# Performance work log

Measured on AMD Instinct MI355X. Metric: run time of the kernel, lower is better.

## Reference

```python
import jax, jax.numpy as jnp
import numpy as np

INPUT_DIM = 64
LATENT_DIM = 512
K = 32
BATCH = 262144


def xavier_uniform(key, shape):
    fan_out, fan_in = shape
    limit = float(np.sqrt(6.0 / (fan_in + fan_out)))
    return jax.random.uniform(key, shape, jnp.float32, -limit, limit)


def setup_inputs() -> dict:
    key = jax.random.key(0)
    kx, ke, kd = jax.random.split(key, 3)
    x = jax.random.normal(kx, (BATCH, INPUT_DIM), dtype=jnp.float32)
    enc_W = xavier_uniform(ke, (LATENT_DIM, INPUT_DIM))  # torch Linear weight layout [out, in]
    enc_b = jnp.zeros((LATENT_DIM,), jnp.float32)
    dec_W = xavier_uniform(kd, (INPUT_DIM, LATENT_DIM))
    dec_b = jnp.zeros((INPUT_DIM,), jnp.float32)
    return {"x": x, "enc_W": enc_W, "enc_b": enc_b, "dec_W": dec_W, "dec_b": dec_b}


def reference(x, enc_W, enc_b, dec_W, dec_b):
    # encode: linear -> relu -> top-k mask
    z = jax.nn.relu(x @ enc_W.T + enc_b)                 # [B, LATENT_DIM]
    vals, idx = jax.lax.top_k(z, K)                      # [B, K]
    rows = jnp.arange(z.shape[0])[:, None]               # [B, 1]
    z_sparse = jnp.zeros_like(z).at[rows, idx].set(vals) # scatter top-k back
    # decode
    x_hat = z_sparse @ dec_W.T + dec_b                   # [B, INPUT_DIM]
    return x_hat, z_sparse
```

## Files before the change

### kernel.cpp

```cpp
#include <hip/hip_runtime.h>


#define BATCH 262144
#define IND   64
#define LAT   512
#define TOPK  32
#define RPB   128
#define TR    32
#define NTT   (RPB / TR)
#define CCAP  128
#define EPSC  4.2e-3f
#define NB    32
#define NBPAD 36

typedef __attribute__((ext_vector_type(8))) short short8;
typedef __attribute__((ext_vector_type(4))) float f32x4;

__device__ __forceinline__ unsigned short f2bf(float f) {
  unsigned u = __float_as_uint(f);
  unsigned r = ((u >> 16) & 1u) + 0x7FFFu;
  return (unsigned short)((u + r) >> 16);
}
__device__ __forceinline__ float bfbits2f(unsigned short s) {
  return __uint_as_float(((unsigned)s) << 16);
}
__device__ __forceinline__ float edgef(int t) {
  return __uint_as_float((unsigned)(1888 + t) << 19);
}
__device__ __forceinline__ short8 pack8(float4 a, float4 b) {
  short8 r;
  r[0] = (short)f2bf(a.x); r[1] = (short)f2bf(a.y);
  r[2] = (short)f2bf(a.z); r[3] = (short)f2bf(a.w);
  r[4] = (short)f2bf(b.x); r[5] = (short)f2bf(b.y);
  r[6] = (short)f2bf(b.z); r[7] = (short)f2bf(b.w);
  return r;
}
__device__ __forceinline__ void split8(const float* p, short8& h, short8& l) {
  #pragma unroll
  for (int i = 0; i < 8; i++) {
    float v = p[i];
    unsigned short hb = f2bf(v);
    float r = v - bfbits2f(hb);
    h[i] = (short)hb;
    l[i] = (short)f2bf(r);
  }
}
__device__ __forceinline__ float exact_dot64(const float* __restrict__ wr,
                                             const float* xr) {
  float4 W[16];
  #pragma unroll
  for (int i = 0; i < 16; i++) W[i] = *(const float4*)(wr + 4*i);
  float s = 0.0f;
  #pragma unroll
  for (int i = 0; i < 16; i++) {
    const float4 xv = *(const float4*)(xr + 4*i);
    s = fmaf(xv.x, W[i].x, s);
    s = fmaf(xv.y, W[i].y, s);
    s = fmaf(xv.z, W[i].z, s);
    s = fmaf(xv.w, W[i].w, s);
  }
  return s;
}

__global__ __launch_bounds__(256, 2)
void sae_fused(const float* __restrict__ xg,
               const float* __restrict__ encW,
               const float* __restrict__ encB,
               const float* __restrict__ decW,
               const float* __restrict__ decB,
               float* __restrict__ out_xhat,
               float* __restrict__ out_z)
{
  __shared__ union {
    unsigned       hist[TR][NBPAD];
    unsigned       fb[256];
    unsigned short cidx[TR][CCAP];
  } hc;
  __shared__ unsigned short zsp[TR][520];
  __shared__ float    xtile[TR][68];
  __shared__ float    rowlo[TR];
  __shared__ float    xabs[TR];
  __shared__ float    xlo0[TR];
  __shared__ float    xinvw[TR];
  __shared__ float    xwid[TR];
  __shared__ int      ccnt[TR];
  __shared__ int      degen[TR];
  __shared__ int      wmax_i;
  __shared__ int      fbmask;

  const int tid  = threadIdx.x;
  const int w    = tid >> 6;
  const int lane = tid & 63;
  const int c    = lane & 15;
  const int q    = lane >> 4;

  if (tid == 0) wmax_i = 0;
  __syncthreads();

  short8 beh[8][2];
  float  lmax = 0.0f;
  #pragma unroll
  for (int n = 0; n < 8; n++)
    #pragma unroll
    for (int ks = 0; ks < 2; ks++) {
      const float* p = encW + (size_t)(128*w + 16*n + c)*IND + 32*ks + 8*q;
      float4 a = *(const float4*)p, b = *(const float4*)(p + 4);
      lmax = fmaxf(lmax, fmaxf(fmaxf(fabsf(a.x), fabsf(a.y)), fmaxf(fabsf(a.z), fabsf(a.w))));
      lmax = fmaxf(lmax, fmaxf(fmaxf(fabsf(b.x), fabsf(b.y)), fmaxf(fabsf(b.z), fabsf(b.w))));
      beh[n][ks] = pack8(a, b);
    }
  atomicMax(&wmax_i, __float_as_int(lmax));

  float ebias[8];
  #pragma unroll
  for (int n = 0; n < 8; n++) ebias[n] = encB[128*w + 16*n + c];
  const float dbias = decB[16*w + c];
  __syncthreads();
  const float wmaxf = __int_as_float(wmax_i);

  #pragma unroll 1
  for (int t = 0; t < NTT; t++) {
    const int rowbase = blockIdx.x * RPB + t * TR;

    {
      uint4 z4 = {0,0,0,0};
      uint4* hp = (uint4*)&hc.hist[0][0];
      hp[tid] = z4;
      if (tid < 32) hp[256 + tid] = z4;
      uint4* zp = (uint4*)&zsp[0][0];
      #pragma unroll
      for (int i = 0; i < 8; i++) zp[tid + 256*i] = z4;
      if (tid < 32) zp[2048 + tid] = z4;
      if (tid < TR) { ccnt[tid] = 0; degen[tid] = 0; }
      if (tid == 0) fbmask = 0;
    }
    {
      const int row = tid >> 3, sub = tid & 7;
      const f32x4* gp = (const f32x4*)(xg + (size_t)(rowbase + row)*IND) + 2*sub;
      f32x4 a = __builtin_nontemporal_load(gp);
      f32x4 b = __builtin_nontemporal_load(gp + 1);
      *(f32x4*)&xtile[row][8*sub]     = a;
      *(f32x4*)&xtile[row][8*sub + 4] = b;
      float s  = fabsf(a.x)+fabsf(a.y)+fabsf(a.z)+fabsf(a.w)
               + fabsf(b.x)+fabsf(b.y)+fabsf(b.z)+fabsf(b.w);
      float s2 = a.x*a.x+a.y*a.y+a.z*a.z+a.w*a.w
               + b.x*b.x+b.y*b.y+b.z*b.z+b.w*b.w;
      s  += __shfl_xor(s, 1);  s  += __shfl_xor(s, 2);  s  += __shfl_xor(s, 4);
      s2 += __shfl_xor(s2, 1); s2 += __shfl_xor(s2, 2); s2 += __shfl_xor(s2, 4);
      if (sub == 0) {
        xabs[row] = s;
        const float sig = 0.058926f * sqrtf(s2);
        xlo0[row]  = fmaxf(0.7f * sig, edgef(1));
        xwid[row]  = (2.5f / (float)NB) * sig;
        xinvw[row] = (float)NB / fmaxf(2.5f * sig, 1e-20f);
      }
    }
    __syncthreads();

    f32x4 acc[2][8];
    #pragma unroll
    for (int m2 = 0; m2 < 2; m2++)
      #pragma unroll
      for (int n = 0; n < 8; n++) acc[m2][n] = (f32x4){0.f,0.f,0.f,0.f};

    #pragma unroll
    for (int m2 = 0; m2 < 2; m2++) {
      const float* xr = &xtile[16*m2 + c][0];
      short8 a0h, a0l, a1h, a1l;
      split8(xr + 8*q,      a0h, a0l);
      split8(xr + 32 + 8*q, a1h, a1l);
      #pragma unroll
      for (int n = 0; n < 8; n++) {
        acc[m2][n] = __builtin_amdgcn_mfma_f32_16x16x32_bf16(a0h, beh[n][0], acc[m2][n], 0,0,0);
        acc[m2][n] = __builtin_amdgcn_mfma_f32_16x16x32_bf16(a0l, beh[n][0], acc[m2][n], 0,0,0);
        acc[m2][n] = __builtin_amdgcn_mfma_f32_16x16x32_bf16(a1h, beh[n][1], acc[m2][n], 0,0,0);
        acc[m2][n] = __builtin_amdgcn_mfma_f32_16x16x32_bf16(a1l, beh[n][1], acc[m2][n], 0,0,0);
      }
    }
    {
      float flo[2][4], fiw[2][4];
      #pragma unroll
      for (int m2 = 0; m2 < 2; m2++)
        #pragma unroll
        for (int r = 0; r < 4; r++) {
          flo[m2][r] = xlo0[16*m2 + 4*q + r];
          fiw[m2][r] = xinvw[16*m2 + 4*q + r];
        }
      #pragma unroll
      for (int m2 = 0; m2 < 2; m2++)
        #pragma unroll
        for (int n = 0; n < 8; n++)
          #pragma unroll
          for (int r = 0; r < 4; r++) {
            float v = fmaxf(acc[m2][n][r] + ebias[n], 0.0f);
            acc[m2][n][r] = v;
            if (v >= flo[m2][r]) {
              const int row = 16*m2 + 4*q + r;
              int k = (int)((v - flo[m2][r]) * fiw[m2][r]);
              k = min(k, NB-1);
              atomicAdd(&hc.hist[row][k], 1u);
            }
          }
    }
    __syncthreads();

    #pragma unroll 1
    for (int rr = 0; rr < 8; rr++) {
      const int row = 8*w + rr;
      uint4 h = {0,0,0,0};
      if (lane < 8) h = *(const uint4*)&hc.hist[row][4*lane];
      int T = (int)(h.x + h.y + h.z + h.w);
      int I = T;
      #pragma unroll
      for (int d = 1; d < 8; d <<= 1) {
        int t2 = __shfl_down(I, d);
        if (lane + d < 8) I += t2;
      }
      const int I0 = __shfl(I, 0);
      if (I0 < TOPK) {
        if (lane == 0) atomicOr(&fbmask, (int)(1u << row));
      } else {
        unsigned long long msk = __ballot(I >= TOPK);
        const int ls = __popcll(msk) - 1;
        const int Il = __shfl(I, ls);
        const int hx = __shfl((int)h.x, ls);
        const int hy = __shfl((int)h.y, ls);
        const int hz = __shfl((int)h.z, ls);
        const int s1 = Il - hx, s2 = s1 - hy, s3 = s2 - hz;
        const int t8 = (s3 >= TOPK) ? 4*ls+3 : (s2 >= TOPK) ? 4*ls+2
                     : (s1 >= TOPK) ? 4*ls+1 : 4*ls;
        if (lane == 0) {
          const float eps2 = EPSC * wmaxf * xabs[row] + 1e-7f;
          rowlo[row] = fmaxf(xlo0[row] + (float)t8 * xwid[row] - 2.0f*eps2, 1e-30f);
        }
      }
    }
    __syncthreads();

    if (fbmask) {
      unsigned* fb = &hc.fb[0];
      unsigned fbm = (unsigned)fbmask;
      while (fbm) {
        const int R = (int)__ffs(fbm) - 1;
        fbm &= fbm - 1;
        fb[tid] = 0;
        __syncthreads();
        if ((lane >> 4) == ((R >> 2) & 3)) {
          const int m2R = R >> 4, rR = R & 3;
          #pragma unroll
          for (int m2 = 0; m2 < 2; m2++)
            #pragma unroll
            for (int r = 0; r < 4; r++)
              if (m2 == m2R && r == rR) {
                #pragma unroll
                for (int n = 0; n < 8; n++) {
                  float v = acc[m2][n][r];
                  int k8 = (int)(__float_as_uint(v) >> 19) - 1888;
                  k8 = max(0, min(255, k8));
                  atomicAdd(&fb[k8], 1u);
                }
              }
        }
        __syncthreads();
        if (w == 0) {
          uint4 h = *(const uint4*)&fb[4*lane];
          int T = (int)(h.x + h.y + h.z + h.w);
          int I = T;
          #pragma unroll
          for (int d = 1; d < 64; d <<= 1) {
            int t2 = __shfl_down(I, d);
            if (lane + d < 64) I += t2;
          }
          const int I0  = __shfl(I, 0);
          const int hx0 = __shfl((int)h.x, 0);
          if (I0 - hx0 < TOPK) {
            if (lane == 0) { degen[R] = 1; rowlo[R] = edgef(1); }
          } else {
            unsigned long long msk = __ballot(I >= TOPK);
            const int ls = __popcll(msk) - 1;
            const int Il = __shfl(I, ls);
            const int hx = __shfl((int)h.x, ls);
            const int hy = __shfl((int)h.y, ls);
            const int hz = __shfl((int)h.z, ls);
            const int s1 = Il - hx, s2 = s1 - hy, s3 = s2 - hz;
            const int t8 = (s3 >= TOPK) ? 4*ls+3 : (s2 >= TOPK) ? 4*ls+2
                         : (s1 >= TOPK) ? 4*ls+1 : 4*ls;
            if (lane == 0) {
              const float eps2 = EPSC * wmaxf * xabs[R] + 1e-7f;
              rowlo[R] = fmaxf(edgef(t8) - 2.0f*eps2, 1e-30f);
            }
          }
        }
        __syncthreads();
      }
    }

    #pragma unroll
    for (int m2 = 0; m2 < 2; m2++)
      #pragma unroll
      for (int r = 0; r < 4; r++) {
        const int row = 16*m2 + 4*q + r;
        const float lo = rowlo[row];
        const int dg = degen[row];
        #pragma unroll
        for (int n = 0; n < 8; n++) {
          const float v = acc[m2][n][r];
          if (v >= lo) {
            if (dg) {
              zsp[row][128*w + 16*n + c] = f2bf(v);
            } else {
              int slot = atomicAdd(&ccnt[row], 1);
              if (slot < CCAP) hc.cidx[row][slot] = (unsigned short)(128*w + 16*n + c);
            }
          }
        }
      }
    __syncthreads();

    #pragma unroll 1
    for (int rr = 0; rr < 8; rr++) {
      const int row = 8*w + rr;
      if (degen[row]) continue;
      const int m  = min(ccnt[row], CCAP);
      const int mA = min(m, 64);
      const int mB = m - mA;
      const float* xr = &xtile[row][0];

      int ciA = 0xFFFF; float sA = -1e30f;
      {
        const int js = (lane < mA) ? (int)hc.cidx[row][lane] : 0;
        float s = exact_dot64(encW + (size_t)js * IND, xr);
        s += encB[js];
        s = fmaxf(s, 0.0f);
        if (lane < mA) { sA = s; ciA = js; }
      }

      if (mB == 0) {
        int rank0 = 0;
        for (int jj = 0; jj < mA; jj++) {
          const float vj = __shfl(sA, jj);
          const int   ij = __shfl(ciA, jj);
          rank0 += (vj > sA || (vj == sA && ij < ciA)) ? 1 : 0;
        }
        if (lane < mA && rank0 < TOPK) zsp[row][ciA] = f2bf(sA);
      } else {
        int ciB = 0xFFFF; float sB = -1e30f;
        {
          const int js = (lane < mB) ? (int)hc.cidx[row][64 + lane] : 0;
          float s = exact_dot64(encW + (size_t)js * IND, xr);
          s += encB[js];
          s = fmaxf(s, 0.0f);
          if (lane < mB) { sB = s; ciB = js; }
        }
        int rank0 = 0, rank1 = 0;
        for (int jj = 0; jj < mA; jj++) {
          const float vj = __shfl(sA, jj);
          const int   ij = __shfl(ciA, jj);
          rank0 += (vj > sA || (vj == sA && ij < ciA)) ? 1 : 0;
          rank1 += (vj > sB || (vj == sB && ij < ciB)) ? 1 : 0;
        }
        for (int jj = 0; jj < mB; jj++) {
          const float vj = __shfl(sB, jj);
          const int   ij = __shfl(ciB, jj);
          rank0 += (vj > sA || (vj == sA && ij < ciA)) ? 1 : 0;
          rank1 += (vj > sB || (vj == sB && ij < ciB)) ? 1 : 0;
        }
        if (lane < mA && rank0 < TOPK) zsp[row][ciA] = f2bf(sA);
        if (lane < mB && rank1 < TOPK) zsp[row][ciB] = f2bf(sB);
      }
    }
    __syncthreads();

    #pragma unroll 1
    for (int rr = 0; rr < 8; rr++) {
      const int row = 8*w + rr;
      const unsigned short* zr = &zsp[row][8*lane];
      f32x4 o0, o1;
      o0.x = bfbits2f(zr[0]); o0.y = bfbits2f(zr[1]); o0.z = bfbits2f(zr[2]); o0.w = bfbits2f(zr[3]);
      o1.x = bfbits2f(zr[4]); o1.y = bfbits2f(zr[5]); o1.z = bfbits2f(zr[6]); o1.w = bfbits2f(zr[7]);
      f32x4* orow = (f32x4*)(out_z + (size_t)(rowbase + row)*LAT + 8*lane);
      __builtin_nontemporal_store(o0, orow);
      __builtin_nontemporal_store(o1, orow + 1);
    }
    {
      f32x4 acc2[2];
      acc2[0] = (f32x4){0.f,0.f,0.f,0.f};
      acc2[1] = (f32x4){0.f,0.f,0.f,0.f};
      const float* pw = decW + (size_t)(16*w + c)*LAT + 8*q;
      #pragma unroll 1
      for (int g = 0; g < 4; g++) {
        short8 bd4[4];
        #pragma unroll
        for (int j = 0; j < 4; j++) {
          const float* p = pw + 32*(4*g + j);
          bd4[j] = pack8(*(const float4*)p, *(const float4*)(p + 4));
        }
        #pragma unroll
        for (int j = 0; j < 4; j++) {
          const int ks = 4*g + j;
          short8 a0 = *(const short8*)&zsp[c][32*ks + 8*q];
          short8 a1 = *(const short8*)&zsp[16 + c][32*ks + 8*q];
          acc2[0] = __builtin_amdgcn_mfma_f32_16x16x32_bf16(a0, bd4[j], acc2[0], 0,0,0);
          acc2[1] = __builtin_amdgcn_mfma_f32_16x16x32_bf16(a1, bd4[j], acc2[1], 0,0,0);
        }
      }
      #pragma unroll
      for (int m2 = 0; m2 < 2; m2++)
        #pragma unroll
        for (int r = 0; r < 4; r++)
          out_xhat[(size_t)(rowbase + 16*m2 + 4*q + r)*IND + 16*w + c] = acc2[m2][r] + dbias;
    }
    __syncthreads();
  }
}

extern "C" void kernel_launch(void* const* d_in, const int* in_sizes, int n_in,
                              void* d_out, int out_size, void* d_ws, size_t ws_size,
                              hipStream_t stream) {
  (void)in_sizes; (void)n_in; (void)out_size; (void)d_ws; (void)ws_size;
  const float* x    = (const float*)d_in[0];
  const float* encW = (const float*)d_in[1];
  const float* encB = (const float*)d_in[2];
  const float* decW = (const float*)d_in[3];
  const float* decB = (const float*)d_in[4];
  float* out_xhat = (float*)d_out;
  float* out_z    = out_xhat + (size_t)BATCH * IND;

  dim3 grid(BATCH / RPB), block(256);
  sae_fused<<<grid, block, 0, stream>>>(x, encW, encB, decW, decB, out_xhat, out_z);
}
```

Before: 1.502 ms.

## Double block to 512 threads, halving per-wave latent columns and rows

Splits the work of each block across 8 waves instead of 4: each wave now holds half the encoder weight fragments and accumulators, processes 4 rows in the per-row top-k phases, and the decoder is split by row-half and column-quarter. Launch bounds move to 512 threads with a higher occupancy target, aiming to cut register use and improve latency hiding. The cost is more waves meeting at each block barrier and redistributed shared-memory initialization.

```diff
diff --git a/kernel.cpp b/kernel.cpp
--- a/kernel.cpp
+++ b/kernel.cpp
@@ -62,7 +62,7 @@
   return s;
 }
 
-__global__ __launch_bounds__(256, 2)
+__global__ __launch_bounds__(512, 4)
 void sae_fused(const float* __restrict__ xg,
                const float* __restrict__ encW,
                const float* __restrict__ encB,
@@ -97,13 +97,13 @@
   if (tid == 0) wmax_i = 0;
   __syncthreads();
 
-  short8 beh[8][2];
+  short8 beh[4][2];
   float  lmax = 0.0f;
   #pragma unroll
-  for (int n = 0; n < 8; n++)
+  for (int n = 0; n < 4; n++)
     #pragma unroll
     for (int ks = 0; ks < 2; ks++) {
-      const float* p = encW + (size_t)(128*w + 16*n + c)*IND + 32*ks + 8*q;
+      const float* p = encW + (size_t)(64*w + 16*n + c)*IND + 32*ks + 8*q;
       float4 a = *(const float4*)p, b = *(const float4*)(p + 4);
       lmax = fmaxf(lmax, fmaxf(fmaxf(fabsf(a.x), fabsf(a.y)), fmaxf(fabsf(a.z), fabsf(a.w))));
       lmax = fmaxf(lmax, fmaxf(fmaxf(fabsf(b.x), fabsf(b.y)), fmaxf(fabsf(b.z), fabsf(b.w))));
@@ -111,10 +111,11 @@
     }
   atomicMax(&wmax_i, __float_as_int(lmax));
 
-  float ebias[8];
+  float ebias[4];
   #pragma unroll
-  for (int n = 0; n < 8; n++) ebias[n] = encB[128*w + 16*n + c];
-  const float dbias = decB[16*w + c];
+  for (int n = 0; n < 4; n++) ebias[n] = encB[64*w + 16*n + c];
+  const int   m2d = w >> 2, wcd = w & 3;
+  const float dbias = decB[16*wcd + c];
   __syncthreads();
   const float wmaxf = __int_as_float(wmax_i);
 
@@ -125,28 +126,25 @@
     {
       uint4 z4 = {0,0,0,0};
       uint4* hp = (uint4*)&hc.hist[0][0];
-      hp[tid] = z4;
-      if (tid < 32) hp[256 + tid] = z4;
+      if (tid < 288) hp[tid] = z4;
       uint4* zp = (uint4*)&zsp[0][0];
       #pragma unroll
-      for (int i = 0; i < 8; i++) zp[tid + 256*i] = z4;
+      for (int i = 0; i < 4; i++) zp[tid + 512*i] = z4;
       if (tid < 32) zp[2048 + tid] = z4;
       if (tid < TR) { ccnt[tid] = 0; degen[tid] = 0; }
       if (tid == 0) fbmask = 0;
     }
     {
-      const int row = tid >> 3, sub = tid & 7;
-      const f32x4* gp = (const f32x4*)(xg + (size_t)(rowbase + row)*IND) + 2*sub;
+      const int row = tid >> 4, sub = tid & 15;
+      const f32x4* gp = (const f32x4*)(xg + (size_t)(rowbase + row)*IND) + sub;
       f32x4 a = __builtin_nontemporal_load(gp);
-      f32x4 b = __builtin_nontemporal_load(gp + 1);
-      *(f32x4*)&xtile[row][8*sub]     = a;
-      *(f32x4*)&xtile[row][8*sub + 4] = b;
-      float s  = fabsf(a.x)+fabsf(a.y)+fabsf(a.z)+fabsf(a.w)
-               + fabsf(b.x)+fabsf(b.y)+fabsf(b.z)+fabsf(b.w);
-      float s2 = a.x*a.x+a.y*a.y+a.z*a.z+a.w*a.w
-               + b.x*b.x+b.y*b.y+b.z*b.z+b.w*b.w;
-      s  += __shfl_xor(s, 1);  s  += __shfl_xor(s, 2);  s  += __shfl_xor(s, 4);
-      s2 += __shfl_xor(s2, 1); s2 += __shfl_xor(s2, 2); s2 += __shfl_xor(s2, 4);
+      *(f32x4*)&xtile[row][4*sub] = a;
+      float s  = fabsf(a.x)+fabsf(a.y)+fabsf(a.z)+fabsf(a.w);
+      float s2 = a.x*a.x+a.y*a.y+a.z*a.z+a.w*a.w;
+      s  += __shfl_xor(s, 1);  s  += __shfl_xor(s, 2);
+      s  += __shfl_xor(s, 4);  s  += __shfl_xor(s, 8);
+      s2 += __shfl_xor(s2, 1); s2 += __shfl_xor(s2, 2);
+      s2 += __shfl_xor(s2, 4); s2 += __shfl_xor(s2, 8);
       if (sub == 0) {
         xabs[row] = s;
         const float sig = 0.058926f * sqrtf(s2);
@@ -157,11 +155,11 @@
     }
     __syncthreads();
 
-    f32x4 acc[2][8];
+    f32x4 acc[2][4];
     #pragma unroll
     for (int m2 = 0; m2 < 2; m2++)
       #pragma unroll
-      for (int n = 0; n < 8; n++) acc[m2][n] = (f32x4){0.f,0.f,0.f,0.f};
+      for (int n = 0; n < 4; n++) acc[m2][n] = (f32x4){0.f,0.f,0.f,0.f};
 
     #pragma unroll
     for (int m2 = 0; m2 < 2; m2++) {
@@ -170,7 +168,7 @@
       split8(xr + 8*q,      a0h, a0l);
       split8(xr + 32 + 8*q, a1h, a1l);
       #pragma unroll
-      for (int n = 0; n < 8; n++) {
+      for (int n = 0; n < 4; n++) {
         acc[m2][n] = __builtin_amdgcn_mfma_f32_16x16x32_bf16(a0h, beh[n][0], acc[m2][n], 0,0,0);
         acc[m2][n] = __builtin_amdgcn_mfma_f32_16x16x32_bf16(a0l, beh[n][0], acc[m2][n], 0,0,0);
         acc[m2][n] = __builtin_amdgcn_mfma_f32_16x16x32_bf16(a1h, beh[n][1], acc[m2][n], 0,0,0);
@@ -189,7 +187,7 @@
       #pragma unroll
       for (int m2 = 0; m2 < 2; m2++)
         #pragma unroll
-        for (int n = 0; n < 8; n++)
+        for (int n = 0; n < 4; n++)
           #pragma unroll
           for (int r = 0; r < 4; r++) {
             float v = fmaxf(acc[m2][n][r] + ebias[n], 0.0f);
@@ -205,8 +203,8 @@
     __syncthreads();
 
     #pragma unroll 1
-    for (int rr = 0; rr < 8; rr++) {
-      const int row = 8*w + rr;
+    for (int rr = 0; rr < 4; rr++) {
+      const int row = 4*w + rr;
       uint4 h = {0,0,0,0};
       if (lane < 8) h = *(const uint4*)&hc.hist[row][4*lane];
       int T = (int)(h.x + h.y + h.z + h.w);
@@ -243,7 +241,7 @@
       while (fbm) {
         const int R = (int)__ffs(fbm) - 1;
         fbm &= fbm - 1;
-        fb[tid] = 0;
+        if (tid < 256) fb[tid] = 0;
         __syncthreads();
         if ((lane >> 4) == ((R >> 2) & 3)) {
           const int m2R = R >> 4, rR = R & 3;
@@ -253,7 +251,7 @@
             for (int r = 0; r < 4; r++)
               if (m2 == m2R && r == rR) {
                 #pragma unroll
-                for (int n = 0; n < 8; n++) {
+                for (int n = 0; n < 4; n++) {
                   float v = acc[m2][n][r];
                   int k8 = (int)(__float_as_uint(v) >> 19) - 1888;
                   k8 = max(0, min(255, k8));
@@ -303,14 +301,14 @@
         const float lo = rowlo[row];
         const int dg = degen[row];
         #pragma unroll
-        for (int n = 0; n < 8; n++) {
+        for (int n = 0; n < 4; n++) {
           const float v = acc[m2][n][r];
           if (v >= lo) {
             if (dg) {
-              zsp[row][128*w + 16*n + c] = f2bf(v);
+              zsp[row][64*w + 16*n + c] = f2bf(v);
             } else {
               int slot = atomicAdd(&ccnt[row], 1);
-              if (slot < CCAP) hc.cidx[row][slot] = (unsigned short)(128*w + 16*n + c);
+              if (slot < CCAP) hc.cidx[row][slot] = (unsigned short)(64*w + 16*n + c);
             }
           }
         }
@@ -318,8 +316,8 @@
     __syncthreads();
 
     #pragma unroll 1
-    for (int rr = 0; rr < 8; rr++) {
-      const int row = 8*w + rr;
+    for (int rr = 0; rr < 4; rr++) {
+      const int row = 4*w + rr;
       if (degen[row]) continue;
       const int m  = min(ccnt[row], CCAP);
       const int mA = min(m, 64);
@@ -372,8 +370,8 @@
     __syncthreads();
 
     #pragma unroll 1
-    for (int rr = 0; rr < 8; rr++) {
-      const int row = 8*w + rr;
+    for (int rr = 0; rr < 4; rr++) {
+      const int row = 4*w + rr;
       const unsigned short* zr = &zsp[row][8*lane];
       f32x4 o0, o1;
       o0.x = bfbits2f(zr[0]); o0.y = bfbits2f(zr[1]); o0.z = bfbits2f(zr[2]); o0.w = bfbits2f(zr[3]);
@@ -383,10 +381,8 @@
       __builtin_nontemporal_store(o1, orow + 1);
     }
     {
-      f32x4 acc2[2];
-      acc2[0] = (f32x4){0.f,0.f,0.f,0.f};
-      acc2[1] = (f32x4){0.f,0.f,0.f,0.f};
-      const float* pw = decW + (size_t)(16*w + c)*LAT + 8*q;
+      f32x4 acc2 = (f32x4){0.f,0.f,0.f,0.f};
+      const float* pw = decW + (size_t)(16*wcd + c)*LAT + 8*q;
       #pragma unroll 1
       for (int g = 0; g < 4; g++) {
         short8 bd4[4];
@@ -398,17 +394,13 @@
         #pragma unroll
         for (int j = 0; j < 4; j++) {
           const int ks = 4*g + j;
-          short8 a0 = *(const short8*)&zsp[c][32*ks + 8*q];
-          short8 a1 = *(const short8*)&zsp[16 + c][32*ks + 8*q];
-          acc2[0] = __builtin_amdgcn_mfma_f32_16x16x32_bf16(a0, bd4[j], acc2[0], 0,0,0);
-          acc2[1] = __builtin_amdgcn_mfma_f32_16x16x32_bf16(a1, bd4[j], acc2[1], 0,0,0);
-        }
-      }
-      #pragma unroll
-      for (int m2 = 0; m2 < 2; m2++)
-        #pragma unroll
-        for (int r = 0; r < 4; r++)
-          out_xhat[(size_t)(rowbase + 16*m2 + 4*q + r)*IND + 16*w + c] = acc2[m2][r] + dbias;
+          short8 a0 = *(const short8*)&zsp[16*m2d + c][32*ks + 8*q];
+          acc2 = __builtin_amdgcn_mfma_f32_16x16x32_bf16(a0, bd4[j], acc2, 0,0,0);
+        }
+      }
+      #pragma unroll
+      for (int r = 0; r < 4; r++)
+        out_xhat[(size_t)(rowbase + 16*m2d + 4*q + r)*IND + 16*wcd + c] = acc2[r] + dbias;
     }
     __syncthreads();
   }
@@ -426,6 +418,6 @@
   float* out_xhat = (float*)d_out;
   float* out_z    = out_xhat + (size_t)BATCH * IND;
 
-  dim3 grid(BATCH / RPB), block(256);
+  dim3 grid(BATCH / RPB), block(512);
   sae_fused<<<grid, block, 0, stream>>>(x, encW, encB, decW, decB, out_xhat, out_z);
 }
```

Result: slower. 1.694 ms (+12.7%).
